# Kernel optimization log

Hardware: AMD Instinct MI355X
Metric: run time of the kernel (lower is better)

The kernel has to match this reference:

```python
import jax, jax.numpy as jnp
import numpy as np

V = 23
EDGES = [(2,1),(3,1),(6,12),(6,10),(6,8),(8,10),(7,13),(7,11),(7,9),(9,11),(2,4),(4,6),(3,5),(5,7),(2,3),(2,14),(3,15),(14,15),(14,16),(15,17),(16,18),(17,19),(18,20),(18,22),(20,22),(19,21),(19,23),(21,23)]
K, H, C, OUT_C = 3, 8, 128, 128
N, T = 32, 256
BN_EPS = 1e-5


def _hop_matrix():
    # binarized union of I, Fw, Bw as in Graph.get_hop_distance
    A = np.zeros((V, V))
    for i, j in EDGES:
        A[i - 1, j - 1] = 1.0
        A[j - 1, i - 1] = 1.0
    np.fill_diagonal(A, 1.0)
    hop = np.full((V, V), V, dtype=np.int32)
    P = np.eye(V)
    for d in range(V):
        reach = P > 0
        hop = np.where(reach & (hop == V), d, hop)  # smallest d with reachability
        P = P @ A
    assert hop.max() < V, 'graph must be connected'
    return hop


def setup_inputs() -> dict:
    key = jax.random.key(0)
    ks = jax.random.split(key, 8)
    hop = _hop_matrix()  # (V,V) int32, max hop = 8 for mediapipe layout
    n_hop = int(hop.max()) + 1
    cin_g = C // H            # 16 in-channels per group
    cout_g = OUT_C // H       # 16 out-channels per group
    return {
        'x': jax.random.normal(ks[0], (N, C, T, V), dtype=jnp.float32),
        'emb_table': jax.random.normal(ks[1], (K, H, n_hop), dtype=jnp.float32) * 0.1,
        'A': jnp.tile(jnp.eye(V, dtype=jnp.float32)[None, None], (K, H, 1, 1))
             + 0.01 * jax.random.normal(ks[2], (K, H, V, V), dtype=jnp.float32),
        'conv_w': jax.random.normal(ks[3], (K * OUT_C, cin_g), dtype=jnp.float32) * 0.05,
        'conv_b': jax.random.normal(ks[4], (K * OUT_C,), dtype=jnp.float32) * 0.05,
        'bn_gamma': jax.random.uniform(ks[5], (OUT_C,), dtype=jnp.float32, minval=0.5, maxval=1.5),
        'bn_beta': jax.random.normal(ks[6], (OUT_C,), dtype=jnp.float32) * 0.1,
        'bn_mean': jax.random.normal(ks[7], (OUT_C,), dtype=jnp.float32) * 0.1,
        'bn_var': jax.random.uniform(jax.random.fold_in(key, 99), (OUT_C,), dtype=jnp.float32, minval=0.5, maxval=1.5),
        'hop': jnp.asarray(hop),
    }


def reference(x, emb_table, A, conv_w, conv_b, bn_gamma, bn_beta, bn_mean, bn_var, hop):
    n, c, t, v = x.shape
    k, h = A.shape[0], A.shape[1]
    cin_g = c // h
    # per-kernel/per-head learned adjacency from hop embedding table
    B = emb_table[:, :, hop]                                   # (k,h,v,v)
    def l2(w):
        return jnp.sqrt(jnp.sum(w * w, axis=-2, keepdims=True)) + 1e-4
    BnA = B / l2(B) + A / l2(A)                                # (k,h,v,v)
    xh = x.reshape(n, h, cin_g, t, v)
    # graph mixing over nodes (k-dim broadcast of x)
    y = jnp.einsum('nhctv,khvw->nkhctw', xh, BnA)              # (n,k,h,c/h,t,v)
    # grouped 1x1 conv (groups = k*h): per (k,h) group 16->16 channel mix
    w = conv_w.reshape(k, h, -1, cin_g)                        # (k,h,out/h,c/h)
    b = conv_b.reshape(k, h, -1)                               # (k,h,out/h)
    y = jnp.einsum('nkhctv,khoc->nkhotv', y, w) + b[None, :, :, :, None, None]
    y = y.reshape(n, k, -1, t, v).sum(axis=1)                  # (n,out_c,t,v)
    # BatchNorm2d (eval mode)
    inv = bn_gamma / jnp.sqrt(bn_var + BN_EPS)
    y = y * inv[None, :, None, None] + (bn_beta - bn_mean * inv)[None, :, None, None]
    # residual is identity (in_channels == out_channels)
    return jax.nn.relu(y + x)
```

## Files before the change

### kernel.cpp

```cpp
#include <hip/hip_runtime.h>
#include <hip/hip_bf16.h>
#include <stdint.h>

#define V 23
#define VP 24
#define KK 3
#define H 8
#define CG 16
#define TDIM 256
#define NB 32
#define TT 64
#define TTM 32
#define OUTC 128
#define CIN 128
#define KDIM 384
#define NSTEP 12
#define NCT 24
#define XROW 392

#define WS_BNA   0
#define WS_SCALE (KK*H*VP*VP)
#define WS_OFFS  (WS_SCALE + OUTC)
#define WS_WT    (WS_OFFS + OUTC)
#define WS_MB    (WS_WT + KK*H*CG*CG)
#define MB_ELEMS ((size_t)H * NSTEP * NCT * 512)
#define WS_NEED_BYTES ((size_t)WS_MB * 4 + MB_ELEMS * 2)

typedef __attribute__((ext_vector_type(8))) short bf16x8;
typedef __attribute__((ext_vector_type(4))) float f32x4;

static __device__ __forceinline__ uint32_t f2bf_rne(float f) {
  uint32_t u = __float_as_uint(f);
  return (u + 0x7fffu + ((u >> 16) & 1u)) >> 16;
}
static __device__ __forceinline__ float bf2f(uint16_t h) {
  return __uint_as_float(((uint32_t)h) << 16);
}

__global__ void prep_fused(const float* __restrict__ emb,
                           const float* __restrict__ A,
                           const float* __restrict__ conv_w,
                           const float* __restrict__ conv_b,
                           const float* __restrict__ gamma,
                           const float* __restrict__ beta,
                           const float* __restrict__ mean,
                           const float* __restrict__ var,
                           const int* __restrict__ hop,
                           int n_hop, float* __restrict__ ws) {
  __shared__ int   hopL[V * V];
  __shared__ float AL[KK][V * V];
  __shared__ float eL[KK][32];
  __shared__ float WtL[KK][CG * CG];
  __shared__ float BnT[KK][VP * VP];
  __shared__ float nbL[KK][V], naL[KK][V];

  const int h = blockIdx.x;
  const int s = blockIdx.y;
  const int tid = threadIdx.x;

  for (int i = tid; i < V * V; i += 256) hopL[i] = hop[i];
  for (int i = tid; i < KK * V * V; i += 256) {
    int k = i / (V * V), r = i % (V * V);
    AL[k][r] = A[((size_t)(k * H + h)) * V * V + r];
  }
  for (int i = tid; i < KK * 32; i += 256) {
    int k = i >> 5, j = i & 31;
    eL[k][j] = (j < n_hop) ? emb[(size_t)(k * H + h) * n_hop + j] : 0.f;
  }
  for (int i = tid; i < KK * CG * CG; i += 256) {
    int o = i & 15, c = (i >> 4) & 15, k = i >> 8;
    WtL[k][c * CG + o] = conv_w[((k * OUTC) + h * CG + o) * CG + c];
  }
  __syncthreads();

  if (tid < KK * V) {
    int k = tid / V, w = tid % V;
    float sb = 0.f, sa = 0.f;
    for (int v = 0; v < V; ++v) {
      float bv = eL[k][hopL[v * V + w]];
      float av = AL[k][v * V + w];
      sb += bv * bv;
      sa += av * av;
    }
    nbL[k][w] = sqrtf(sb) + 1e-4f;
    naL[k][w] = sqrtf(sa) + 1e-4f;
  } else if (s == 0 && tid >= 192 && tid < 192 + CG) {
    int oc = h * CG + (tid - 192);
    float inv = gamma[oc] * rsqrtf(var[oc] + 1e-5f);
    float sb = conv_b[oc] + conv_b[OUTC + oc] + conv_b[2 * OUTC + oc];
    ws[WS_SCALE + oc] = inv;
    ws[WS_OFFS + oc] = beta[oc] - mean[oc] * inv + sb * inv;
  }
  __syncthreads();

  for (int i = tid; i < KK * VP * VP; i += 256) {
    int k = i / (VP * VP), r = i % (VP * VP);
    int w = r / VP, v = r % VP;
    float val = 0.f;
    if (v < V && w < V)
      val = eL[k][hopL[v * V + w]] / nbL[k][w] + AL[k][v * V + w] / naL[k][w];
    BnT[k][w * VP + v] = val;
  }
  __syncthreads();

  uint16_t* mb = (uint16_t*)(ws + WS_MB);
  for (int idx = tid; idx < NCT * 64; idx += 256) {
    int lane = idx & 63, ct = idx >> 6;
    int col = ct * 16 + (lane & 15);
    int o = col / VP, w = col - o * VP;
    int q = lane >> 4;
    int k0 = s * 32 + q * 8;
    int ci = k0 / VP, v0 = k0 - ci * VP;
    float wt0 = WtL[0][ci * CG + o];
    float wt1 = WtL[1][ci * CG + o];
    float wt2 = WtL[2][ci * CG + o];
    const float* b0 = &BnT[0][w * VP + v0];
    const float* b1 = &BnT[1][w * VP + v0];
    const float* b2 = &BnT[2][w * VP + v0];
    uint32_t packed[4];
#pragma unroll
    for (int jj = 0; jj < 4; ++jj) {
      float vlo = 0.f, vhi = 0.f;
      int j0 = jj * 2, j1 = jj * 2 + 1;
      if (w < V) {
        if (v0 + j0 < V) vlo = wt0 * b0[j0] + wt1 * b1[j0] + wt2 * b2[j0];
        if (v0 + j1 < V) vhi = wt0 * b0[j1] + wt1 * b1[j1] + wt2 * b2[j1];
      }
      packed[jj] = f2bf_rne(vlo) | (f2bf_rne(vhi) << 16);
    }
    *(uint4*)&mb[((size_t)(h * NSTEP + s) * NCT + ct) * 512 + lane * 8] =
        make_uint4(packed[0], packed[1], packed[2], packed[3]);
  }
}

__global__ void prep1_kernel(const float* __restrict__ emb,
                             const float* __restrict__ A,
                             const float* __restrict__ conv_w,
                             const float* __restrict__ conv_b,
                             const float* __restrict__ gamma,
                             const float* __restrict__ beta,
                             const float* __restrict__ mean,
                             const float* __restrict__ var,
                             const int* __restrict__ hop,
                             int n_hop, float* __restrict__ ws) {
  int b = blockIdx.x;
  int tid = threadIdx.x;
  if (b < KK * H) {
    __shared__ float nbv[VP], nav[VP];
    const float* e = emb + b * n_hop;
    const float* a = A + b * V * V;
    if (tid < VP) {
      float nb = 1.f, na = 1.f;
      if (tid < V) {
        float sb = 0.f, sa = 0.f;
        for (int v = 0; v < V; ++v) {
          float bv = e[hop[v * V + tid]];
          float av = a[v * V + tid];
          sb += bv * bv;
          sa += av * av;
        }
        nb = sqrtf(sb) + 1e-4f;
        na = sqrtf(sa) + 1e-4f;
      }
      nbv[tid] = nb;
      nav[tid] = na;
    }
    __syncthreads();
    float* dst = ws + WS_BNA + b * VP * VP;
    for (int idx = tid; idx < VP * VP; idx += 256) {
      int v = idx / VP, w = idx % VP;
      float val = 0.f;
      if (v < V && w < V)
        val = e[hop[v * V + w]] / nbv[w] + a[v * V + w] / nav[w];
      dst[idx] = val;
    }
  } else if (b == KK * H) {
    if (tid < OUTC) {
      float inv = gamma[tid] * rsqrtf(var[tid] + 1e-5f);
      float sb = conv_b[tid] + conv_b[OUTC + tid] + conv_b[2 * OUTC + tid];
      ws[WS_SCALE + tid] = inv;
      ws[WS_OFFS + tid] = beta[tid] - mean[tid] * inv + sb * inv;
    }
  } else {
    int idx = (b - KK * H - 1) * 256 + tid;
    if (idx < KK * H * CG * CG) {
      int o = idx & 15, c = (idx >> 4) & 15, h = (idx >> 8) & 7, k = idx >> 11;
      ws[WS_WT + ((k * H + h) * CG + c) * CG + o] =
          conv_w[((k * OUTC) + h * CG + o) * CG + c];
    }
  }
}

__global__ __launch_bounds__(256, 4) void gcn_main_mfma(
    const float* __restrict__ x,
    const float* __restrict__ ws,
    float* __restrict__ out) {
  __shared__ __align__(16) uint16_t Xa[TTM * XROW];

  const int tid = threadIdx.x;
  const int t0 = blockIdx.x * TTM;
  const int h  = blockIdx.y;
  const int n  = blockIdx.z;

  for (int u = tid; u < CG * TTM * 6; u += 256) {
    int c = u / (TTM * 6);
    int r = u % (TTM * 6);
    int tt = r / 6, vc = r % 6;
    const float* xrow =
        x + ((size_t)((n * CIN + h * CG + c) * TDIM) + (t0 + tt)) * V;
    float f0 = xrow[vc * 4 + 0];
    float f1 = xrow[vc * 4 + 1];
    float f2 = xrow[vc * 4 + 2];
    float f3 = (vc < 5) ? xrow[vc * 4 + 3] : 0.f;
    uint32_t lo = f2bf_rne(f0) | (f2bf_rne(f1) << 16);
    uint32_t hi = f2bf_rne(f2) | (f2bf_rne(f3) << 16);
    *(uint2*)&Xa[tt * XROW + c * VP + vc * 4] = make_uint2(lo, hi);
  }
  __syncthreads();

  const int wave = tid >> 6, lane = tid & 63;
  const int m = lane & 15, q = lane >> 4;

  const uint16_t* mb = (const uint16_t*)(ws + WS_MB) +
                       ((size_t)h * NSTEP * NCT + wave * 6) * 512 + lane * 8;

  f32x4 acc[2][6];
#pragma unroll
  for (int rt = 0; rt < 2; ++rt)
#pragma unroll
    for (int c6 = 0; c6 < 6; ++c6) acc[rt][c6] = (f32x4){0.f, 0.f, 0.f, 0.f};

  for (int s = 0; s < NSTEP; ++s) {
    bf16x8 bf[6];
#pragma unroll
    for (int c6 = 0; c6 < 6; ++c6)
      bf[c6] = *(const bf16x8*)(mb + (size_t)(s * NCT + c6) * 512);
    bf16x8 af[2];
#pragma unroll
    for (int rt = 0; rt < 2; ++rt)
      af[rt] = *(const bf16x8*)&Xa[(rt * 16 + m) * XROW + s * 32 + q * 8];
#pragma unroll
    for (int c6 = 0; c6 < 6; ++c6)
#pragma unroll
      for (int rt = 0; rt < 2; ++rt)
        acc[rt][c6] = __builtin_amdgcn_mfma_f32_16x16x32_bf16(
            af[rt], bf[c6], acc[rt][c6], 0, 0, 0);
  }

#pragma unroll
  for (int c6 = 0; c6 < 6; ++c6) {
    int col = (wave * 6 + c6) * 16 + m;
    int o = col / VP, w = col - o * VP;
    float sc = ws[WS_SCALE + h * CG + o];
    float of = ws[WS_OFFS + h * CG + o];
    bool valid = (w < V);
    float* obase =
        out + ((size_t)(n * OUTC + h * CG + o) * TDIM + t0) * V + w;
#pragma unroll
    for (int rt = 0; rt < 2; ++rt) {
#pragma unroll
      for (int reg = 0; reg < 4; ++reg) {
        int row = rt * 16 + q * 4 + reg;
        float resid = bf2f(Xa[row * XROW + col]);
        float y = fmaf(acc[rt][c6][reg], sc, of) + resid;
        if (valid) obase[(size_t)row * V] = fmaxf(y, 0.f);
      }
    }
  }
}

__global__ __launch_bounds__(256, 3) void gcn_main_valu(
    const float* __restrict__ x,
    const float* __restrict__ ws,
    float* __restrict__ out) {
  __shared__ __align__(16) uint16_t Xs[CG * TT * VP];

  const int tid = threadIdx.x;
  const int t0 = blockIdx.x * TT;
  const int h  = blockIdx.y;
  const int n  = blockIdx.z;

  for (int u = tid; u < CG * TT * 6; u += 256) {
    int c = u / (TT * 6);
    int r = u % (TT * 6);
    int tt = r / 6, vc = r % 6;
    const float* xrow =
        x + ((size_t)((n * CIN + h * CG + c) * TDIM) + (t0 + tt)) * V;
    float f0 = xrow[vc * 4 + 0];
    float f1 = xrow[vc * 4 + 1];
    float f2 = xrow[vc * 4 + 2];
    float f3 = (vc < 5) ? xrow[vc * 4 + 3] : 0.f;
    uint32_t lo = f2bf_rne(f0) | (f2bf_rne(f1) << 16);
    uint32_t hi = f2bf_rne(f2) | (f2bf_rne(f3) << 16);
    *(uint2*)&Xs[(c * TT + tt) * VP + vc * 4] = make_uint2(lo, hi);
  }
  __syncthreads();

  const int oq = __builtin_amdgcn_readfirstlane(tid >> 6);
  const int tt = tid & 63;

  const float* wt  = ws + WS_WT  + ((size_t)h * CG * CG);
  const float* bna = ws + WS_BNA + ((size_t)h * VP * VP);

  float acc[4][VP];
#pragma unroll
  for (int o = 0; o < 4; ++o)
#pragma unroll
    for (int w = 0; w < VP; ++w) acc[o][w] = 0.f;

  for (int k = 0; k < KK; ++k) {
    const float* wtk  = wt  + (size_t)k * H * CG * CG;
    const float* bnak = bna + (size_t)k * H * VP * VP;
    for (int vb = 0; vb < 3; ++vb) {
      float xwv[4][8];
#pragma unroll
      for (int o = 0; o < 4; ++o)
#pragma unroll
        for (int j = 0; j < 8; ++j) xwv[o][j] = 0.f;
#pragma unroll 4
      for (int c = 0; c < CG; ++c) {
        uint4 raw = *(const uint4*)&Xs[(c * TT + tt) * VP + vb * 8];
        float4 wv = *(const float4*)&wtk[c * CG + (oq << 2)];
        float xv[8];
        xv[0] = __uint_as_float(raw.x << 16);
        xv[1] = __uint_as_float(raw.x & 0xffff0000u);
        xv[2] = __uint_as_float(raw.y << 16);
        xv[3] = __uint_as_float(raw.y & 0xffff0000u);
        xv[4] = __uint_as_float(raw.z << 16);
        xv[5] = __uint_as_float(raw.z & 0xffff0000u);
        xv[6] = __uint_as_float(raw.w << 16);
        xv[7] = __uint_as_float(raw.w & 0xffff0000u);
#pragma unroll
        for (int o = 0; o < 4; ++o) {
          float wo = (&wv.x)[o];
#pragma unroll
          for (int j = 0; j < 8; ++j) xwv[o][j] = fmaf(wo, xv[j], xwv[o][j]);
        }
      }
#pragma unroll
      for (int j = 0; j < 8; ++j) {
        const int v = vb * 8 + j;
        const float* bnrow = &bnak[v * VP];
#pragma unroll
        for (int wb = 0; wb < 6; ++wb) {
          float4 bn = *(const float4*)(bnrow + wb * 4);
#pragma unroll
          for (int o = 0; o < 4; ++o) {
            acc[o][wb * 4 + 0] = fmaf(xwv[o][j], bn.x, acc[o][wb * 4 + 0]);
            acc[o][wb * 4 + 1] = fmaf(xwv[o][j], bn.y, acc[o][wb * 4 + 1]);
            acc[o][wb * 4 + 2] = fmaf(xwv[o][j], bn.z, acc[o][wb * 4 + 2]);
            acc[o][wb * 4 + 3] = fmaf(xwv[o][j], bn.w, acc[o][wb * 4 + 3]);
          }
        }
      }
    }
  }

#pragma unroll
  for (int o = 0; o < 4; ++o) {
    int og = (oq << 2) + o;
    int oc = h * CG + og;
    float sc = ws[WS_SCALE + oc];
    float of = ws[WS_OFFS + oc];
    float* orow = out + ((size_t)(n * OUTC + oc) * TDIM + (t0 + tt)) * V;
    const uint16_t* xsrow = &Xs[(og * TT + tt) * VP];
#pragma unroll
    for (int w = 0; w < V; ++w) {
      float resid = bf2f(xsrow[w]);
      float y = fmaf(acc[o][w], sc, of) + resid;
      orow[w] = fmaxf(y, 0.f);
    }
  }
}

extern "C" void kernel_launch(void* const* d_in, const int* in_sizes, int n_in,
                              void* d_out, int out_size, void* d_ws, size_t ws_size,
                              hipStream_t stream) {
  const float* x      = (const float*)d_in[0];
  const float* emb    = (const float*)d_in[1];
  const float* A      = (const float*)d_in[2];
  const float* conv_w = (const float*)d_in[3];
  const float* conv_b = (const float*)d_in[4];
  const float* gamma  = (const float*)d_in[5];
  const float* beta   = (const float*)d_in[6];
  const float* mean   = (const float*)d_in[7];
  const float* var    = (const float*)d_in[8];
  const int*   hop    = (const int*)d_in[9];
  float* ws  = (float*)d_ws;
  float* out = (float*)d_out;

  int n_hop = in_sizes[1] / (KK * H);

  if (ws_size >= WS_NEED_BYTES) {
    prep_fused<<<dim3(H, NSTEP), dim3(256), 0, stream>>>(
        emb, A, conv_w, conv_b, gamma, beta, mean, var, hop, n_hop, ws);
    gcn_main_mfma<<<dim3(TDIM / TTM, H, NB), dim3(256), 0, stream>>>(x, ws, out);
  } else {
    prep1_kernel<<<dim3(KK * H + 1 + 24), dim3(256), 0, stream>>>(
        emb, A, conv_w, conv_b, gamma, beta, mean, var, hop, n_hop, ws);
    gcn_main_valu<<<dim3(TDIM / TT, H, NB), dim3(256), 0, stream>>>(x, ws, out);
  }
}
```

Baseline: 243.3 us.

## Software-pipeline B-fragment global loads with four register buffers in MFMA loop

Fully unrolls the 12-step MFMA loop and prefetches the precomputed B fragments two steps ahead into four rotating register buffers. The first two steps' loads are issued before the X staging into shared memory, so their latency overlaps the staging. This is meant to hide global-load latency in the main loop. The extra registers force launch bounds down from 4 to 3 blocks per SIMD, which lowers occupancy.

```diff
diff --git a/kernel.cpp b/kernel.cpp
--- a/kernel.cpp
+++ b/kernel.cpp
@@ -191,7 +191,28 @@
   }
 }
 
-__global__ __launch_bounds__(256, 4) void gcn_main_mfma(
+#define LOADB(arr, s_)                                                     \
+  {                                                                        \
+    _Pragma("unroll")                                                      \
+    for (int c6 = 0; c6 < 6; ++c6)                                         \
+      arr[c6] = *(const bf16x8*)(mb + (size_t)((s_) * NCT + c6) * 512);    \
+  }
+
+#define STEPB(arr, s_)                                                     \
+  {                                                                        \
+    bf16x8 af[2];                                                          \
+    _Pragma("unroll")                                                      \
+    for (int rt = 0; rt < 2; ++rt)                                         \
+      af[rt] = *(const bf16x8*)&Xa[(rt * 16 + m) * XROW + (s_) * 32 + q * 8]; \
+    _Pragma("unroll")                                                      \
+    for (int c6 = 0; c6 < 6; ++c6)                                         \
+      _Pragma("unroll")                                                    \
+      for (int rt = 0; rt < 2; ++rt)                                       \
+        acc[rt][c6] = __builtin_amdgcn_mfma_f32_16x16x32_bf16(             \
+            af[rt], arr[c6], acc[rt][c6], 0, 0, 0);                        \
+  }
+
+__global__ __launch_bounds__(256, 3) void gcn_main_mfma(
     const float* __restrict__ x,
     const float* __restrict__ ws,
     float* __restrict__ out) {
@@ -201,6 +222,16 @@
   const int t0 = blockIdx.x * TTM;
   const int h  = blockIdx.y;
   const int n  = blockIdx.z;
+
+  const int wave = tid >> 6, lane = tid & 63;
+  const int m = lane & 15, q = lane >> 4;
+
+  const uint16_t* mb = (const uint16_t*)(ws + WS_MB) +
+                       ((size_t)h * NSTEP * NCT + wave * 6) * 512 + lane * 8;
+
+  bf16x8 bA[6], bB[6], bC[6], bD[6];
+  LOADB(bA, 0);
+  LOADB(bB, 1);
 
   for (int u = tid; u < CG * TTM * 6; u += 256) {
     int c = u / (TTM * 6);
@@ -218,34 +249,34 @@
   }
   __syncthreads();
 
-  const int wave = tid >> 6, lane = tid & 63;
-  const int m = lane & 15, q = lane >> 4;
-
-  const uint16_t* mb = (const uint16_t*)(ws + WS_MB) +
-                       ((size_t)h * NSTEP * NCT + wave * 6) * 512 + lane * 8;
-
   f32x4 acc[2][6];
 #pragma unroll
   for (int rt = 0; rt < 2; ++rt)
 #pragma unroll
     for (int c6 = 0; c6 < 6; ++c6) acc[rt][c6] = (f32x4){0.f, 0.f, 0.f, 0.f};
 
-  for (int s = 0; s < NSTEP; ++s) {
-    bf16x8 bf[6];
-#pragma unroll
-    for (int c6 = 0; c6 < 6; ++c6)
-      bf[c6] = *(const bf16x8*)(mb + (size_t)(s * NCT + c6) * 512);
-    bf16x8 af[2];
-#pragma unroll
-    for (int rt = 0; rt < 2; ++rt)
-      af[rt] = *(const bf16x8*)&Xa[(rt * 16 + m) * XROW + s * 32 + q * 8];
-#pragma unroll
-    for (int c6 = 0; c6 < 6; ++c6)
-#pragma unroll
-      for (int rt = 0; rt < 2; ++rt)
-        acc[rt][c6] = __builtin_amdgcn_mfma_f32_16x16x32_bf16(
-            af[rt], bf[c6], acc[rt][c6], 0, 0, 0);
-  }
+  LOADB(bC, 2);
+  LOADB(bD, 3);
+  STEPB(bA, 0);
+  STEPB(bB, 1);
+  LOADB(bA, 4);
+  LOADB(bB, 5);
+  STEPB(bC, 2);
+  STEPB(bD, 3);
+  LOADB(bC, 6);
+  LOADB(bD, 7);
+  STEPB(bA, 4);
+  STEPB(bB, 5);
+  LOADB(bA, 8);
+  LOADB(bB, 9);
+  STEPB(bC, 6);
+  STEPB(bD, 7);
+  LOADB(bC, 10);
+  LOADB(bD, 11);
+  STEPB(bA, 8);
+  STEPB(bB, 9);
+  STEPB(bC, 10);
+  STEPB(bD, 11);
 
 #pragma unroll
   for (int c6 = 0; c6 < 6; ++c6) {
```

New measurement: 227.7 us. 1.07x faster.
